# Optimization experiments

Hardware: AMD Instinct MI355X
Metric: run time of the kernel (lower is better)

The kernel has to match this reference:

```python
import jax, jax.numpy as jnp
import numpy as np

EMBED_DIM = 1024
NUM_HEADS = 16
HEAD_DIM = EMBED_DIM // NUM_HEADS


def setup_inputs() -> dict:
    key = jax.random.key(0)
    ks = jax.random.split(key, 5)
    x = jax.random.normal(ks[0], (2, 2048, EMBED_DIM), dtype=jnp.float32)
    s_in = 1.0 / np.sqrt(EMBED_DIM)
    W_qkv = jax.random.uniform(ks[1], (EMBED_DIM, 3 * EMBED_DIM), minval=-s_in, maxval=s_in, dtype=jnp.float32)
    b_qkv = jax.random.uniform(ks[2], (3 * EMBED_DIM,), minval=-s_in, maxval=s_in, dtype=jnp.float32)
    W_out = jax.random.uniform(ks[3], (EMBED_DIM, EMBED_DIM), minval=-s_in, maxval=s_in, dtype=jnp.float32)
    b_out = jax.random.uniform(ks[4], (EMBED_DIM,), minval=-s_in, maxval=s_in, dtype=jnp.float32)
    return {"x": x, "W_qkv": W_qkv, "b_qkv": b_qkv, "W_out": W_out, "b_out": b_out}


def reference(x, W_qkv, b_qkv, W_out, b_out):
    B, S, D = x.shape
    H, Dh = NUM_HEADS, HEAD_DIM
    qkv = x @ W_qkv + b_qkv                       # [B, S, 3D]
    q, k, v = jnp.split(qkv, 3, axis=-1)
    # [B, S, D] -> [B, H, S, Dh]
    q = q.reshape(B, S, H, Dh).transpose(0, 2, 1, 3)
    k = k.reshape(B, S, H, Dh).transpose(0, 2, 1, 3)
    v = v.reshape(B, S, H, Dh).transpose(0, 2, 1, 3)
    scores = jnp.einsum('bhqd,bhkd->bhqk', q, k) / jnp.sqrt(jnp.float32(Dh))
    probs = jax.nn.softmax(scores, axis=-1)       # [B, H, S, S]
    attn = jnp.einsum('bhqk,bhkd->bhqd', probs, v)
    attn = attn.transpose(0, 2, 1, 3).reshape(B, S, D)
    return attn @ W_out + b_out
```

## Files before the change

kernel.cpp:

```cpp
#include <hip/hip_runtime.h>
#include <hip/hip_bf16.h>

#define DEV __device__ __forceinline__

typedef __bf16 bf16x8 __attribute__((ext_vector_type(8)));
typedef float f32x4 __attribute__((ext_vector_type(4)));
typedef float f32x16 __attribute__((ext_vector_type(16)));
using u16 = unsigned short;
using u32 = unsigned int;

static constexpr int S = 2048;
static constexpr int D = 1024;
static constexpr float SCQ = 0.125f * 1.44269504088896340736f;

DEV u16 f2bf(float f) {
  unsigned u = __builtin_bit_cast(unsigned, f);
  u += 0x7fffu + ((u >> 16) & 1u);
  return (u16)(u >> 16);
}
DEV u16 f2bfr(float f) {
  return (u16)((__builtin_bit_cast(u32, f) + 0x8000u) >> 16);
}
DEV u32 pk2(float a, float b) {
  u32 ua = __builtin_bit_cast(u32, a) + 0x8000u;
  u32 ub = __builtin_bit_cast(u32, b) + 0x8000u;
  return __builtin_amdgcn_perm(ub, ua, 0x07060302);
}

DEV void gl16(const u16* __restrict__ g, u16* l) {
  __builtin_amdgcn_global_load_lds((const __attribute__((address_space(1))) u32*)g,
                                   (__attribute__((address_space(3))) u32*)l, 16, 0, 0);
}

__global__ __launch_bounds__(256) void k_prep(const float* __restrict__ x, u16* __restrict__ Xb,
                                              const float* __restrict__ Wqkv, u16* __restrict__ WqkvT,
                                              const float* __restrict__ Wout, u16* __restrict__ WoutT) {
  __shared__ float t[32][33];
  const int bid = blockIdx.x;
  const int tid = threadIdx.x;
  if (bid < 4096) {
    const int i = bid * 256 + tid;
    const float4 v = reinterpret_cast<const float4*>(x)[i];
    ushort4 o;
    o.x = f2bf(v.x); o.y = f2bf(v.y); o.z = f2bf(v.z); o.w = f2bf(v.w);
    reinterpret_cast<ushort4*>(Xb)[i] = o;
    return;
  }
  const float* in;
  u16* out;
  int R, C, bx, by;
  if (bid < 4096 + 3072) {
    const int b = bid - 4096;
    in = Wqkv; out = WqkvT; R = 1024; C = 3072;
    bx = b % 96; by = b / 96;
  } else {
    const int b = bid - 7168;
    in = Wout; out = WoutT; R = 1024; C = 1024;
    bx = b & 31; by = b >> 5;
  }
  const int tx = tid & 31, ty = tid >> 5;
  const int c0 = bx * 32, r0 = by * 32;
  for (int i = ty; i < 32; i += 8)
    t[i][tx] = in[(size_t)(r0 + i) * C + c0 + tx];
  __syncthreads();
  for (int i = ty; i < 32; i += 8)
    out[(size_t)(c0 + i) * R + r0 + tx] = f2bf(t[tx][i]);
}

template <int MODE, int TN>
__global__ __launch_bounds__(256) void k_gemm(const u16* __restrict__ A, const u16* __restrict__ Bt,
                                              const float* __restrict__ bias, int M, int N, int K,
                                              u16* __restrict__ Qb, u16* __restrict__ Kb,
                                              u16* __restrict__ Vt, float* __restrict__ outF) {
  constexpr int NJ = TN / 32;
  __shared__ u16 As[128][32];
  __shared__ u16 Bs[TN][32];
  const int tid = threadIdx.x;
  const int lane = tid & 63, wave = tid >> 6;
  const int l15 = lane & 15, quad = lane >> 4;
  const int m0 = blockIdx.y * 128, n0 = blockIdx.x * TN;
  const int wm = (wave >> 1) * 64, wn = (wave & 1) * (TN / 2);
  const int lr = lane >> 2;
  const int lcs = ((((lane & 3) - (lane >> 3)) & 3)) * 8;
  const int sq = ((quad + (l15 >> 1)) & 3) * 8;

  f32x4 acc[4][NJ];
#pragma unroll
  for (int i = 0; i < 4; i++)
#pragma unroll
    for (int j = 0; j < NJ; j++) acc[i][j] = (f32x4){0.f, 0.f, 0.f, 0.f};

  const u16* Aw0 = &A[(size_t)(m0 + wave * 32 + lr) * K + lcs];
  const u16* Aw1 = &A[(size_t)(m0 + wave * 32 + 16 + lr) * K + lcs];
  const u16* Bw0;
  const u16* Bw1;
  if constexpr (TN == 128) {
    Bw0 = &Bt[(size_t)(n0 + wave * 32 + lr) * K + lcs];
    Bw1 = &Bt[(size_t)(n0 + wave * 32 + 16 + lr) * K + lcs];
  } else {
    Bw0 = &Bt[(size_t)(n0 + wave * 16 + lr) * K + lcs];
  }

  for (int kk = 0; kk < K; kk += 32) {
    gl16(Aw0 + kk, &As[wave * 32][0]);
    gl16(Aw1 + kk, &As[wave * 32 + 16][0]);
    if constexpr (TN == 128) {
      gl16(Bw0 + kk, &Bs[wave * 32][0]);
      gl16(Bw1 + kk, &Bs[wave * 32 + 16][0]);
    } else {
      gl16(Bw0 + kk, &Bs[wave * 16][0]);
    }
    __syncthreads();
    bf16x8 af[4], bfv[NJ];
#pragma unroll
    for (int i = 0; i < 4; i++)
      af[i] = *reinterpret_cast<const bf16x8*>(&As[wm + i * 16 + l15][sq]);
#pragma unroll
    for (int j = 0; j < NJ; j++)
      bfv[j] = *reinterpret_cast<const bf16x8*>(&Bs[wn + j * 16 + l15][sq]);
#pragma unroll
    for (int i = 0; i < 4; i++)
#pragma unroll
      for (int j = 0; j < NJ; j++)
        acc[i][j] = __builtin_amdgcn_mfma_f32_16x16x32_bf16(af[i], bfv[j], acc[i][j], 0, 0, 0);
    __syncthreads();
  }

  if constexpr (MODE == 0) {
    __shared__ u16 LT[64][136];
    if (n0 >= 2048) {
      const int b = m0 >> 11, sbase = m0 & 2047;
#pragma unroll
      for (int p = 0; p < 2; p++) {
        __syncthreads();
        if ((wave & 1) == p) {
#pragma unroll
          for (int j = 0; j < NJ; j++) {
            const int n = n0 + wn + j * 16 + l15;
            const float vb = bias[n];
#pragma unroll
            for (int i = 0; i < 4; i++) {
              uint2 pw;
              pw.x = pk2(acc[i][j][0] + vb, acc[i][j][1] + vb);
              pw.y = pk2(acc[i][j][2] + vb, acc[i][j][3] + vb);
              *reinterpret_cast<uint2*>(&LT[j * 16 + l15][wm + i * 16 + quad * 4]) = pw;
            }
          }
        }
        __syncthreads();
        const int h = ((n0 - 2048) >> 6) + p;
        const int bh = b * 16 + h;
        const int nl = tid >> 2, cc = (tid & 3) * 32;
        u16* dst = &Vt[((size_t)bh * 64 + nl) * S + sbase + cc];
#pragma unroll
        for (int k = 0; k < 4; k++)
          reinterpret_cast<uint4*>(dst)[k] = *reinterpret_cast<const uint4*>(&LT[nl][cc + k * 8]);
      }
    } else {
#pragma unroll
      for (int i = 0; i < 4; i++) {
#pragma unroll
        for (int j = 0; j < NJ; j++) {
#pragma unroll
          for (int r = 0; r < 4; r++) {
            const int m = m0 + wm + i * 16 + quad * 4 + r;
            const int n = n0 + wn + j * 16 + l15;
            const float v = acc[i][j][r] + bias[n];
            const int h = (n >> 6) & 15, dh = n & 63;
            const int b = m >> 11, s = m & 2047;
            const int bh = b * 16 + h;
            if (n < 1024) Qb[((size_t)bh * S + s) * 64 + dh] = f2bfr(v * SCQ);
            else          Kb[((size_t)bh * S + s) * 64 + dh] = f2bfr(v);
          }
        }
      }
    }
  } else {
#pragma unroll
    for (int i = 0; i < 4; i++)
#pragma unroll
      for (int j = 0; j < NJ; j++)
#pragma unroll
        for (int r = 0; r < 4; r++) {
          const int m = m0 + wm + i * 16 + quad * 4 + r;
          const int n = n0 + wn + j * 16 + l15;
          outF[(size_t)m * N + n] = acc[i][j][r] + bias[n];
        }
  }
}

__global__ __launch_bounds__(256, 2) void k_attn(const u16* __restrict__ Qb,
                                                 const u16* __restrict__ Kb,
                                                 const u16* __restrict__ Vt,
                                                 u16* __restrict__ attnB) {
  __shared__ u16 Ks[64][72];
  __shared__ u16 Vs[64][72];
  __shared__ u16 Pl[4][32][72];
  const int bh = blockIdx.y;
  const int q0 = blockIdx.x * 128;
  const int tid = threadIdx.x;
  const int lane = tid & 63, wave = tid >> 6;
  const int l31 = lane & 31, hi = lane >> 5;
  const u16* Qh = Qb + (size_t)bh * S * 64;
  const u16* Kh = Kb + (size_t)bh * S * 64;
  const u16* Vh = Vt + (size_t)bh * 64 * S;
  const int qrow = q0 + wave * 32 + l31;
  bf16x8 qf[4];
#pragma unroll
  for (int f = 0; f < 4; f++)
    qf[f] = *reinterpret_cast<const bf16x8*>(&Qh[(size_t)qrow * 64 + f * 16 + hi * 8]);

  const int r0 = tid >> 3, c0 = (tid & 7) * 8;

  float li = 0.f;
  f32x16 o0, o1;
#pragma unroll
  for (int r = 0; r < 16; r++) { o0[r] = 0.f; o1[r] = 0.f; }

  uint4 pk0 = *reinterpret_cast<const uint4*>(&Kh[(size_t)r0 * 64 + c0]);
  uint4 pk1 = *reinterpret_cast<const uint4*>(&Kh[(size_t)(r0 + 32) * 64 + c0]);
  uint4 pv0 = *reinterpret_cast<const uint4*>(&Vh[(size_t)r0 * S + c0]);
  uint4 pv1 = *reinterpret_cast<const uint4*>(&Vh[(size_t)(r0 + 32) * S + c0]);

  for (int kb = 0; kb < S / 64; kb++) {
    __syncthreads();
    *reinterpret_cast<uint4*>(&Ks[r0][c0]) = pk0;
    *reinterpret_cast<uint4*>(&Ks[r0 + 32][c0]) = pk1;
    *reinterpret_cast<uint4*>(&Vs[r0][c0]) = pv0;
    *reinterpret_cast<uint4*>(&Vs[r0 + 32][c0]) = pv1;
    __syncthreads();
    if (kb + 1 < S / 64) {
      const u16* Kn = Kh + (size_t)(kb + 1) * 64 * 64;
      pk0 = *reinterpret_cast<const uint4*>(&Kn[(size_t)r0 * 64 + c0]);
      pk1 = *reinterpret_cast<const uint4*>(&Kn[(size_t)(r0 + 32) * 64 + c0]);
      pv0 = *reinterpret_cast<const uint4*>(&Vh[(size_t)r0 * S + (kb + 1) * 64 + c0]);
      pv1 = *reinterpret_cast<const uint4*>(&Vh[(size_t)(r0 + 32) * S + (kb + 1) * 64 + c0]);
    }
    f32x16 z[2];
#pragma unroll
    for (int kt = 0; kt < 2; kt++) {
#pragma unroll
      for (int r = 0; r < 16; r++) z[kt][r] = 0.f;
#pragma unroll
      for (int f = 0; f < 4; f++) {
        const bf16x8 a = *reinterpret_cast<const bf16x8*>(&Ks[kt * 32 + l31][f * 16 + hi * 8]);
        z[kt] = __builtin_amdgcn_mfma_f32_32x32x16_bf16(a, qf[f], z[kt], 0, 0, 0);
      }
    }
    float s0 = 0.f, s1 = 0.f, s2 = 0.f, s3 = 0.f;
#pragma unroll
    for (int kt = 0; kt < 2; kt++)
#pragma unroll
      for (int r = 0; r < 16; r++) {
        const float p = __builtin_amdgcn_exp2f(z[kt][r]);
        z[kt][r] = p;
        if ((r & 3) == 0) s0 += p; else if ((r & 3) == 1) s1 += p;
        else if ((r & 3) == 2) s2 += p; else s3 += p;
      }
    li += (s0 + s1) + (s2 + s3);
#pragma unroll
    for (int kt = 0; kt < 2; kt++)
#pragma unroll
      for (int g = 0; g < 4; g++) {
        uint2 pw;
        pw.x = pk2(z[kt][g * 4 + 0], z[kt][g * 4 + 1]);
        pw.y = pk2(z[kt][g * 4 + 2], z[kt][g * 4 + 3]);
        *reinterpret_cast<uint2*>(&Pl[wave][l31][kt * 32 + g * 8 + hi * 4]) = pw;
      }
#pragma unroll
    for (int f = 0; f < 4; f++) {
      const bf16x8 bp = *reinterpret_cast<const bf16x8*>(&Pl[wave][l31][f * 16 + hi * 8]);
      const bf16x8 av0 = *reinterpret_cast<const bf16x8*>(&Vs[l31][f * 16 + hi * 8]);
      const bf16x8 av1 = *reinterpret_cast<const bf16x8*>(&Vs[32 + l31][f * 16 + hi * 8]);
      o0 = __builtin_amdgcn_mfma_f32_32x32x16_bf16(av0, bp, o0, 0, 0, 0);
      o1 = __builtin_amdgcn_mfma_f32_32x32x16_bf16(av1, bp, o1, 0, 0, 0);
    }
  }
  li += __shfl_xor(li, 32);
  const float inv = 1.f / li;
#pragma unroll
  for (int dt = 0; dt < 2; dt++) {
    const f32x16& od = dt ? o1 : o0;
#pragma unroll
    for (int g = 0; g < 4; g++) {
      uint2 ow;
      ow.x = pk2(od[g * 4 + 0] * inv, od[g * 4 + 1] * inv);
      ow.y = pk2(od[g * 4 + 2] * inv, od[g * 4 + 3] * inv);
      *reinterpret_cast<uint2*>(&Pl[wave][l31][dt * 32 + g * 8 + hi * 4]) = ow;
    }
  }
  const int b = bh >> 4, h = bh & 15;
  const int mbase = b * S + q0 + wave * 32;
  const int qr = lane >> 1, ch = (lane & 1) * 32;
  u16* dst = &attnB[(size_t)(mbase + qr) * D + h * 64 + ch];
#pragma unroll
  for (int c = 0; c < 4; c++)
    reinterpret_cast<uint4*>(dst)[c] = *reinterpret_cast<const uint4*>(&Pl[wave][qr][ch + c * 8]);
}

extern "C" void kernel_launch(void* const* d_in, const int* in_sizes, int n_in,
                              void* d_out, int out_size, void* d_ws, size_t ws_size,
                              hipStream_t stream) {
  const float* x = (const float*)d_in[0];
  const float* Wqkv = (const float*)d_in[1];
  const float* bqkv = (const float*)d_in[2];
  const float* Wout = (const float*)d_in[3];
  const float* bout = (const float*)d_in[4];
  float* out = (float*)d_out;

  char* p = (char*)d_ws;
  u16* Xb = (u16*)p;    p += (size_t)4096 * 1024 * 2;
  u16* WqkvT = (u16*)p; p += (size_t)3072 * 1024 * 2;
  u16* WoutT = (u16*)p; p += (size_t)1024 * 1024 * 2;
  u16* Qb = (u16*)p;    p += (size_t)32 * 2048 * 64 * 2;
  u16* Kb = (u16*)p;    p += (size_t)32 * 2048 * 64 * 2;
  u16* Vt = (u16*)p;    p += (size_t)32 * 64 * 2048 * 2;
  u16* attnB = (u16*)p; p += (size_t)4096 * 1024 * 2;

  k_prep<<<4096 + 3072 + 1024, 256, 0, stream>>>(x, Xb, Wqkv, WqkvT, Wout, WoutT);
  k_gemm<0, 128><<<dim3(3072 / 128, 4096 / 128), 256, 0, stream>>>(
      Xb, WqkvT, bqkv, 4096, 3072, 1024, Qb, Kb, Vt, nullptr);
  k_attn<<<dim3(2048 / 128, 32), 256, 0, stream>>>(Qb, Kb, Vt, attnB);
  k_gemm<1, 64><<<dim3(1024 / 64, 4096 / 128), 256, 0, stream>>>(
      attnB, WoutT, bout, 4096, 1024, 1024, nullptr, nullptr, nullptr, out);
}
```

Baseline: 205.7 us.

## Double-buffer LDS tiles in GEMM to overlap global loads with MFMA

The GEMM kernel now keeps two LDS buffers for the A and B tiles. It issues the direct-to-LDS loads for the next K slice right after the barrier, then runs MFMAs on the current slice, which drops one of the two barriers per iteration. The goal is to hide global load latency behind compute in the QKV and output projections. The cost is double the LDS footprint for these tiles, which may lower occupancy. Correctness also relies on the barrier waiting for the outstanding async loads.

```diff
diff --git a/kernel.cpp b/kernel.cpp
--- a/kernel.cpp
+++ b/kernel.cpp
@@ -73,8 +73,8 @@
                                               u16* __restrict__ Qb, u16* __restrict__ Kb,
                                               u16* __restrict__ Vt, float* __restrict__ outF) {
   constexpr int NJ = TN / 32;
-  __shared__ u16 As[128][32];
-  __shared__ u16 Bs[TN][32];
+  __shared__ u16 As[2][128][32];
+  __shared__ u16 Bs[2][TN][32];
   const int tid = threadIdx.x;
   const int lane = tid & 63, wave = tid >> 6;
   const int l15 = lane & 15, quad = lane >> 4;
@@ -101,29 +101,41 @@
     Bw0 = &Bt[(size_t)(n0 + wave * 16 + lr) * K + lcs];
   }
 
-  for (int kk = 0; kk < K; kk += 32) {
-    gl16(Aw0 + kk, &As[wave * 32][0]);
-    gl16(Aw1 + kk, &As[wave * 32 + 16][0]);
-    if constexpr (TN == 128) {
-      gl16(Bw0 + kk, &Bs[wave * 32][0]);
-      gl16(Bw1 + kk, &Bs[wave * 32 + 16][0]);
-    } else {
-      gl16(Bw0 + kk, &Bs[wave * 16][0]);
-    }
+  gl16(Aw0, &As[0][wave * 32][0]);
+  gl16(Aw1, &As[0][wave * 32 + 16][0]);
+  if constexpr (TN == 128) {
+    gl16(Bw0, &Bs[0][wave * 32][0]);
+    gl16(Bw1, &Bs[0][wave * 32 + 16][0]);
+  } else {
+    gl16(Bw0, &Bs[0][wave * 16][0]);
+  }
+
+  int cur = 0;
+#pragma unroll 2
+  for (int kk = 0; kk < K; kk += 32, cur ^= 1) {
     __syncthreads();
+    if (kk + 32 < K) {
+      gl16(Aw0 + kk + 32, &As[cur ^ 1][wave * 32][0]);
+      gl16(Aw1 + kk + 32, &As[cur ^ 1][wave * 32 + 16][0]);
+      if constexpr (TN == 128) {
+        gl16(Bw0 + kk + 32, &Bs[cur ^ 1][wave * 32][0]);
+        gl16(Bw1 + kk + 32, &Bs[cur ^ 1][wave * 32 + 16][0]);
+      } else {
+        gl16(Bw0 + kk + 32, &Bs[cur ^ 1][wave * 16][0]);
+      }
+    }
     bf16x8 af[4], bfv[NJ];
 #pragma unroll
     for (int i = 0; i < 4; i++)
-      af[i] = *reinterpret_cast<const bf16x8*>(&As[wm + i * 16 + l15][sq]);
+      af[i] = *reinterpret_cast<const bf16x8*>(&As[cur][wm + i * 16 + l15][sq]);
 #pragma unroll
     for (int j = 0; j < NJ; j++)
-      bfv[j] = *reinterpret_cast<const bf16x8*>(&Bs[wn + j * 16 + l15][sq]);
+      bfv[j] = *reinterpret_cast<const bf16x8*>(&Bs[cur][wn + j * 16 + l15][sq]);
 #pragma unroll
     for (int i = 0; i < 4; i++)
 #pragma unroll
       for (int j = 0; j < NJ; j++)
         acc[i][j] = __builtin_amdgcn_mfma_f32_16x16x32_bf16(af[i], bfv[j], acc[i][j], 0, 0, 0);
-    __syncthreads();
   }
 
   if constexpr (MODE == 0) {
```

Result: no change. 202.5 us (-1.6%).
